# Performance work log

Hardware: AMD Instinct MI355X
Metric: run time of the kernel (lower is better)

The kernel has to match this reference:

```python
import jax, jax.numpy as jnp
import numpy as np

N_NODES = 50000
N_EDGES = 600000
D = 128
HIDDEN = 128
N_GRAPHS = 128
N_CLASSES = 10
N_STACKED = 3  # num_layers - 1


def setup_inputs() -> dict:
    key = jax.random.key(0)
    ks = jax.random.split(key, 12)
    s = 1.0 / np.sqrt(HIDDEN)
    inp = {
        "x": jax.random.normal(ks[0], (N_NODES, D), dtype=jnp.float32),
        "edge_index": jax.random.randint(ks[1], (2, N_EDGES), 0, N_NODES, dtype=jnp.int64),
        "batch": jnp.sort(jax.random.randint(ks[2], (N_NODES,), 0, N_GRAPHS, dtype=jnp.int64)),
        "W1": jax.random.normal(ks[3], (D, HIDDEN), dtype=jnp.float32) * s,
        "R1": jax.random.normal(ks[4], (D, HIDDEN), dtype=jnp.float32) * s,
        "b1": jnp.zeros((HIDDEN,), dtype=jnp.float32),
        "Wc": jax.random.normal(ks[5], (N_STACKED, HIDDEN, HIDDEN), dtype=jnp.float32) * s,
        "Rc": jax.random.normal(ks[6], (N_STACKED, HIDDEN, HIDDEN), dtype=jnp.float32) * s,
        "bc": jnp.zeros((N_STACKED, HIDDEN), dtype=jnp.float32),
        "lin1_w": jax.random.normal(ks[7], (HIDDEN, HIDDEN), dtype=jnp.float32) * s,
        "lin1_b": jnp.zeros((HIDDEN,), dtype=jnp.float32),
        "lin2_w": jax.random.normal(ks[8], (HIDDEN, N_CLASSES), dtype=jnp.float32) * s,
        "lin2_b": jnp.zeros((N_CLASSES,), dtype=jnp.float32),
    }
    return inp


def _gcn_norm(edge_index, n_nodes):
    # symmetric GCN normalization coeffs per edge (edge_weight=None -> ones)
    src, dst = edge_index[0], edge_index[1]
    ones = jnp.ones((edge_index.shape[1],), dtype=jnp.float32)
    deg = jax.ops.segment_sum(ones, dst, num_segments=n_nodes)
    dinv = jnp.where(deg > 0, jax.lax.rsqrt(jnp.maximum(deg, 1.0)), 0.0)
    return dinv[src] * dinv[dst]


def _gcs(x, src, dst, norm, W, R, b):
    # GCN aggregation on transformed features + linear skip (root) connection
    h = x @ W                                   # [N, H]
    msg = h[src] * norm[:, None]                # gather + scale, [E, H]
    agg = jax.ops.segment_sum(msg, dst, num_segments=x.shape[0])
    return agg + x @ R + b


def reference(x, edge_index, batch, W1, R1, b1, Wc, Rc, bc,
              lin1_w, lin1_b, lin2_w, lin2_b):
    src, dst = edge_index[0], edge_index[1]
    norm = _gcn_norm(edge_index, x.shape[0])

    h = jax.nn.relu(_gcs(x, src, dst, norm, W1, R1, b1))
    for i in range(N_STACKED):
        h = jax.nn.relu(_gcs(h, src, dst, norm, Wc[i], Rc[i], bc[i]))
    last = h

    # global mean pool over graphs
    sums = jax.ops.segment_sum(h, batch, num_segments=N_GRAPHS)
    cnts = jax.ops.segment_sum(jnp.ones((h.shape[0],), h.dtype), batch,
                               num_segments=N_GRAPHS)
    pooled = sums / jnp.maximum(cnts, 1.0)[:, None]

    g = jax.nn.relu(pooled @ lin1_w + lin1_b)   # dropout is identity in eval mode
    logits = g @ lin2_w + lin2_b
    return jax.nn.log_softmax(logits, axis=-1), last
```

## Files before the change

### kernel.cpp

```cpp
#include <hip/hip_runtime.h>

#define N_NODES  50000
#define N_EDGES  600000
#define DIM      128
#define N_GRAPHS 128
#define N_CLASSES 10
#define NB_SCAN  196
#define LDSW     136
#define NZB      8204


typedef __bf16 bf16x8 __attribute__((ext_vector_type(8)));
typedef float  f32x4  __attribute__((ext_vector_type(4)));

__device__ inline unsigned short f2bf(float f) {
  union { float f; unsigned int i; } u; u.f = f;
  unsigned int r = u.i + 0x7fff + ((u.i >> 16) & 1);
  return (unsigned short)(r >> 16);
}
__device__ inline float bf2f(unsigned short s) {
  union { unsigned int i; float f; } u; u.i = ((unsigned int)s) << 16;
  return u.f;
}
__device__ inline bf16x8 pack8(float4 lo, float4 hi) {
  union { bf16x8 v; unsigned short s[8]; } u;
  u.s[0] = f2bf(lo.x); u.s[1] = f2bf(lo.y); u.s[2] = f2bf(lo.z); u.s[3] = f2bf(lo.w);
  u.s[4] = f2bf(hi.x); u.s[5] = f2bf(hi.y); u.s[6] = f2bf(hi.z); u.s[7] = f2bf(hi.w);
  return u.v;
}


__global__ __launch_bounds__(256) void k_prep(float* __restrict__ zbase,
                                              const float* __restrict__ W1,
                                              const float* __restrict__ R1,
                                              const float* __restrict__ Wc,
                                              const float* __restrict__ Rc,
                                              unsigned short* __restrict__ pk) {
  if (blockIdx.x < NZB) {
    int i = blockIdx.x * 256 + threadIdx.x;
    if (i < 2100000) zbase[i] = 0.f;
    return;
  }
  int pb = blockIdx.x - NZB;
  int mm = pb >> 3, sub = pb & 7;
  const float* src = (mm == 0) ? W1
                   : (mm < 4)  ? Wc + (size_t)(mm - 1) * DIM * DIM
                   : (mm == 4) ? R1
                               : Rc + (size_t)(mm - 5) * DIM * DIM;
  int idx = sub * 256 + threadIdx.x;
  int lane = idx & 63;
  int kc   = (idx >> 6) & 3;
  int nt   = idx >> 8;
  int col  = nt * 16 + (lane & 15);
  int k0   = kc * 32 + (lane >> 4) * 8;
  unsigned short* dst = pk + (size_t)mm * 16384 + (size_t)idx * 8;
  ushort4 u;
  u.x = f2bf(src[(k0 + 0) * DIM + col]);
  u.y = f2bf(src[(k0 + 1) * DIM + col]);
  u.z = f2bf(src[(k0 + 2) * DIM + col]);
  u.w = f2bf(src[(k0 + 3) * DIM + col]);
  *(ushort4*)&dst[0] = u;
  u.x = f2bf(src[(k0 + 4) * DIM + col]);
  u.y = f2bf(src[(k0 + 5) * DIM + col]);
  u.z = f2bf(src[(k0 + 6) * DIM + col]);
  u.w = f2bf(src[(k0 + 7) * DIM + col]);
  *(ushort4*)&dst[4] = u;
}


__global__ __launch_bounds__(256) void k_deg(const int* __restrict__ ei,
                                             int* __restrict__ deg) {
  int e = blockIdx.x * 256 + threadIdx.x;
  if (e < N_EDGES) atomicAdd(&deg[ei[N_EDGES + e]], 1);
}

__global__ __launch_bounds__(256) void k_dinvsum(const int* __restrict__ deg,
                                                 float* __restrict__ dinv,
                                                 int* __restrict__ bsum) {
  int i = blockIdx.x * 256 + threadIdx.x;
  int t = threadIdx.x;
  int d = (i < N_NODES) ? deg[i] : 0;
  if (i < N_NODES) dinv[i] = (d > 0) ? rsqrtf((float)d) : 0.f;
  int dp = (d + 7) & ~7;
  __shared__ int tmp[256];
  tmp[t] = dp;
  __syncthreads();
  for (int off = 128; off > 0; off >>= 1) {
    if (t < off) tmp[t] += tmp[t + off];
    __syncthreads();
  }
  if (t == 0) bsum[blockIdx.x] = tmp[0];
}

__global__ __launch_bounds__(256) void k_bscan(const int* __restrict__ bsum,
                                               int* __restrict__ boff,
                                               int* __restrict__ rowp) {
  int t = threadIdx.x;
  int v = (t < NB_SCAN) ? bsum[t] : 0;
  __shared__ int tmp[256];
  tmp[t] = v;
  __syncthreads();
  for (int off = 1; off < 256; off <<= 1) {
    int add = (t >= off) ? tmp[t - off] : 0;
    __syncthreads();
    tmp[t] += add;
    __syncthreads();
  }
  boff[t] = tmp[t] - v;
  if (t == 255) rowp[N_NODES] = tmp[255];
}

__global__ __launch_bounds__(256) void k_rowp(const int* __restrict__ deg,
                                              const int* __restrict__ boff,
                                              int* __restrict__ rowp) {
  int i = blockIdx.x * 256 + threadIdx.x;
  int t = threadIdx.x;
  int dp = (i < N_NODES) ? ((deg[i] + 7) & ~7) : 0;
  __shared__ int tmp[256];
  tmp[t] = dp;
  __syncthreads();
  for (int off = 1; off < 256; off <<= 1) {
    int add = (t >= off) ? tmp[t - off] : 0;
    __syncthreads();
    tmp[t] += add;
    __syncthreads();
  }
  if (i < N_NODES) rowp[i] = boff[blockIdx.x] + tmp[t] - dp;
}

__global__ __launch_bounds__(256) void k_fill(const int* __restrict__ ei,
                                              const int* __restrict__ rowp,
                                              int* __restrict__ cnt,
                                              const float* __restrict__ dinv,
                                              int* __restrict__ csrc,
                                              float* __restrict__ enorm) {
  int e = blockIdx.x * 256 + threadIdx.x;
  if (e < N_EDGES) {
    int s = ei[e];
    int d = ei[N_EDGES + e];
    int p = rowp[d] + atomicAdd(&cnt[d], 1);
    csrc[p] = s;
    enorm[p] = dinv[s] * dinv[d];
  }
}


__global__ __launch_bounds__(256) void k_gemm0(const float* __restrict__ xf,
                                               const unsigned short* __restrict__ pkW,
                                               const unsigned short* __restrict__ pkR,
                                               const float* __restrict__ bv,
                                               unsigned short* __restrict__ hwb,
                                               unsigned short* __restrict__ skipb) {
  const int tid  = threadIdx.x;
  const int wave = tid >> 6, lane = tid & 63;
  const int m = lane & 15, q = lane >> 4;
  const int rbase = blockIdx.x * 64 + wave * 16;
  const int arow  = rbase + m;
  const bool aok  = arow < N_NODES;

  bf16x8 a[4];
#pragma unroll
  for (int kc = 0; kc < 4; ++kc) {
    float4 lo = make_float4(0.f, 0.f, 0.f, 0.f);
    float4 hi = make_float4(0.f, 0.f, 0.f, 0.f);
    if (aok) {
      lo = *(const float4*)&xf[arow * DIM + kc * 32 + q * 8];
      hi = *(const float4*)&xf[arow * DIM + kc * 32 + q * 8 + 4];
    }
    a[kc] = pack8(lo, hi);
  }

  f32x4 acc[16];
#pragma unroll
  for (int t = 0; t < 16; ++t) acc[t] = (f32x4){0.f, 0.f, 0.f, 0.f};

#pragma unroll
  for (int nt = 0; nt < 8; ++nt) {
    const unsigned short* pw = pkW + ((size_t)(nt * 4) * 64 + lane) * 8;
    const unsigned short* pr = pkR + ((size_t)(nt * 4) * 64 + lane) * 8;
#pragma unroll
    for (int kc = 0; kc < 4; ++kc) {
      bf16x8 bW = *(const bf16x8*)(pw + (size_t)kc * 64 * 8);
      acc[nt] = __builtin_amdgcn_mfma_f32_16x16x32_bf16(a[kc], bW, acc[nt], 0, 0, 0);
    }
#pragma unroll
    for (int kc = 0; kc < 4; ++kc) {
      bf16x8 bR = *(const bf16x8*)(pr + (size_t)kc * 64 * 8);
      acc[8 + nt] = __builtin_amdgcn_mfma_f32_16x16x32_bf16(a[kc], bR, acc[8 + nt], 0, 0, 0);
    }
  }

#pragma unroll
  for (int nt = 0; nt < 8; ++nt) {
    int col = nt * 16 + m;
    float bias = bv[col];
#pragma unroll
    for (int rg = 0; rg < 4; ++rg) {
      int row = rbase + q * 4 + rg;
      if (row < N_NODES) {
        hwb[row * DIM + col]   = f2bf(acc[nt][rg]);
        skipb[row * DIM + col] = f2bf(acc[8 + nt][rg] + bias);
      }
    }
  }
}


template<bool LAST>
__global__ __launch_bounds__(256) void k_aggemm(const unsigned short* __restrict__ hin,
                                                const int* __restrict__ rowp,
                                                const int* __restrict__ csrc,
                                                const float* __restrict__ enorm,
                                                const unsigned short* __restrict__ pkW,
                                                const unsigned short* __restrict__ pkR,
                                                const float* __restrict__ bv,
                                                unsigned short* __restrict__ hout,
                                                unsigned short* __restrict__ skipb,
                                                float* __restrict__ skipf) {
  __shared__ unsigned short xs[64 * LDSW];
  const int tid = threadIdx.x;
  const int row0 = blockIdx.x * 64;

  {
    int hw = tid >> 5;
    int l4 = (tid & 31) * 4;
    for (int rnd = 0; rnd < 8; ++rnd) {
      int n = row0 + rnd * 8 + hw;
      float4 acc = make_float4(0.f, 0.f, 0.f, 0.f);
      if (n < N_NODES) {
        ushort4 s = *(const ushort4*)&skipb[n * DIM + l4];
        acc = make_float4(bf2f(s.x), bf2f(s.y), bf2f(s.z), bf2f(s.w));
        int e0 = rowp[n], e1 = rowp[n + 1];
        for (int e = e0; e < e1; e += 8) {
          int4   csA = *(const int4*)&csrc[e];
          int4   csB = *(const int4*)&csrc[e + 4];
          float4 wvA = *(const float4*)&enorm[e];
          float4 wvB = *(const float4*)&enorm[e + 4];
          ushort4 u0 = *(const ushort4*)&hin[csA.x * DIM + l4];
          ushort4 u1 = *(const ushort4*)&hin[csA.y * DIM + l4];
          ushort4 u2 = *(const ushort4*)&hin[csA.z * DIM + l4];
          ushort4 u3 = *(const ushort4*)&hin[csA.w * DIM + l4];
          ushort4 u4 = *(const ushort4*)&hin[csB.x * DIM + l4];
          ushort4 u5 = *(const ushort4*)&hin[csB.y * DIM + l4];
          ushort4 u6 = *(const ushort4*)&hin[csB.z * DIM + l4];
          ushort4 u7 = *(const ushort4*)&hin[csB.w * DIM + l4];
          acc.x = fmaf(wvA.x, bf2f(u0.x), fmaf(wvA.y, bf2f(u1.x), fmaf(wvA.z, bf2f(u2.x), fmaf(wvA.w, bf2f(u3.x), acc.x))));
          acc.x = fmaf(wvB.x, bf2f(u4.x), fmaf(wvB.y, bf2f(u5.x), fmaf(wvB.z, bf2f(u6.x), fmaf(wvB.w, bf2f(u7.x), acc.x))));
          acc.y = fmaf(wvA.x, bf2f(u0.y), fmaf(wvA.y, bf2f(u1.y), fmaf(wvA.z, bf2f(u2.y), fmaf(wvA.w, bf2f(u3.y), acc.y))));
          acc.y = fmaf(wvB.x, bf2f(u4.y), fmaf(wvB.y, bf2f(u5.y), fmaf(wvB.z, bf2f(u6.y), fmaf(wvB.w, bf2f(u7.y), acc.y))));
          acc.z = fmaf(wvA.x, bf2f(u0.z), fmaf(wvA.y, bf2f(u1.z), fmaf(wvA.z, bf2f(u2.z), fmaf(wvA.w, bf2f(u3.z), acc.z))));
          acc.z = fmaf(wvB.x, bf2f(u4.z), fmaf(wvB.y, bf2f(u5.z), fmaf(wvB.z, bf2f(u6.z), fmaf(wvB.w, bf2f(u7.z), acc.z))));
          acc.w = fmaf(wvA.x, bf2f(u0.w), fmaf(wvA.y, bf2f(u1.w), fmaf(wvA.z, bf2f(u2.w), fmaf(wvA.w, bf2f(u3.w), acc.w))));
          acc.w = fmaf(wvB.x, bf2f(u4.w), fmaf(wvB.y, bf2f(u5.w), fmaf(wvB.z, bf2f(u6.w), fmaf(wvB.w, bf2f(u7.w), acc.w))));
        }
        acc.x = fmaxf(acc.x, 0.f);
        acc.y = fmaxf(acc.y, 0.f);
        acc.z = fmaxf(acc.z, 0.f);
        acc.w = fmaxf(acc.w, 0.f);
      }
      int r = rnd * 8 + hw;
      ushort4 o;
      o.x = f2bf(acc.x); o.y = f2bf(acc.y); o.z = f2bf(acc.z); o.w = f2bf(acc.w);
      *(ushort4*)&xs[r * LDSW + l4] = o;
    }
  }
  __syncthreads();

  const int wave = tid >> 6, lane = tid & 63;
  const int m = lane & 15, q = lane >> 4;
  const int rbase = row0 + wave * 16;

  bf16x8 a[4];
#pragma unroll
  for (int kc = 0; kc < 4; ++kc)
    a[kc] = *(const bf16x8*)&xs[(wave * 16 + m) * LDSW + kc * 32 + q * 8];

  f32x4 acc[16];
#pragma unroll
  for (int t = 0; t < 16; ++t) acc[t] = (f32x4){0.f, 0.f, 0.f, 0.f};

#pragma unroll
  for (int nt = 0; nt < 8; ++nt) {
    const unsigned short* pw = pkW + ((size_t)(nt * 4) * 64 + lane) * 8;
    const unsigned short* pr = pkR + ((size_t)(nt * 4) * 64 + lane) * 8;
#pragma unroll
    for (int kc = 0; kc < 4; ++kc) {
      bf16x8 bW = *(const bf16x8*)(pw + (size_t)kc * 64 * 8);
      acc[nt] = __builtin_amdgcn_mfma_f32_16x16x32_bf16(a[kc], bW, acc[nt], 0, 0, 0);
    }
#pragma unroll
    for (int kc = 0; kc < 4; ++kc) {
      bf16x8 bR = *(const bf16x8*)(pr + (size_t)kc * 64 * 8);
      acc[8 + nt] = __builtin_amdgcn_mfma_f32_16x16x32_bf16(a[kc], bR, acc[8 + nt], 0, 0, 0);
    }
  }

#pragma unroll
  for (int nt = 0; nt < 8; ++nt) {
    int col = nt * 16 + m;
    float bias = bv[col];
#pragma unroll
    for (int rg = 0; rg < 4; ++rg) {
      int row = rbase + q * 4 + rg;
      if (row < N_NODES) {
        hout[row * DIM + col] = f2bf(acc[nt][rg]);
        float v = acc[8 + nt][rg] + bias;
        if (LAST) skipf[row * DIM + col] = v;
        else      skipb[row * DIM + col] = f2bf(v);
      }
    }
  }
}


__global__ __launch_bounds__(256) void k_aggF(const unsigned short* __restrict__ hwb,
                                              const int* __restrict__ rowp,
                                              const int* __restrict__ csrc,
                                              const float* __restrict__ enorm,
                                              float* __restrict__ actf) {
  int n = blockIdx.x * 8 + (threadIdx.x >> 5);
  if (n >= N_NODES) return;
  int l4 = (threadIdx.x & 31) * 4;
  float4 acc = *(const float4*)&actf[n * DIM + l4];
  int e0 = rowp[n], e1 = rowp[n + 1];
  for (int e = e0; e < e1; e += 8) {
    int4   csA = *(const int4*)&csrc[e];
    int4   csB = *(const int4*)&csrc[e + 4];
    float4 wvA = *(const float4*)&enorm[e];
    float4 wvB = *(const float4*)&enorm[e + 4];
    ushort4 u0 = *(const ushort4*)&hwb[csA.x * DIM + l4];
    ushort4 u1 = *(const ushort4*)&hwb[csA.y * DIM + l4];
    ushort4 u2 = *(const ushort4*)&hwb[csA.z * DIM + l4];
    ushort4 u3 = *(const ushort4*)&hwb[csA.w * DIM + l4];
    ushort4 u4 = *(const ushort4*)&hwb[csB.x * DIM + l4];
    ushort4 u5 = *(const ushort4*)&hwb[csB.y * DIM + l4];
    ushort4 u6 = *(const ushort4*)&hwb[csB.z * DIM + l4];
    ushort4 u7 = *(const ushort4*)&hwb[csB.w * DIM + l4];
    acc.x = fmaf(wvA.x, bf2f(u0.x), fmaf(wvA.y, bf2f(u1.x), fmaf(wvA.z, bf2f(u2.x), fmaf(wvA.w, bf2f(u3.x), acc.x))));
    acc.x = fmaf(wvB.x, bf2f(u4.x), fmaf(wvB.y, bf2f(u5.x), fmaf(wvB.z, bf2f(u6.x), fmaf(wvB.w, bf2f(u7.x), acc.x))));
    acc.y = fmaf(wvA.x, bf2f(u0.y), fmaf(wvA.y, bf2f(u1.y), fmaf(wvA.z, bf2f(u2.y), fmaf(wvA.w, bf2f(u3.y), acc.y))));
    acc.y = fmaf(wvB.x, bf2f(u4.y), fmaf(wvB.y, bf2f(u5.y), fmaf(wvB.z, bf2f(u6.y), fmaf(wvB.w, bf2f(u7.y), acc.y))));
    acc.z = fmaf(wvA.x, bf2f(u0.z), fmaf(wvA.y, bf2f(u1.z), fmaf(wvA.z, bf2f(u2.z), fmaf(wvA.w, bf2f(u3.z), acc.z))));
    acc.z = fmaf(wvB.x, bf2f(u4.z), fmaf(wvB.y, bf2f(u5.z), fmaf(wvB.z, bf2f(u6.z), fmaf(wvB.w, bf2f(u7.z), acc.z))));
    acc.w = fmaf(wvA.x, bf2f(u0.w), fmaf(wvA.y, bf2f(u1.w), fmaf(wvA.z, bf2f(u2.w), fmaf(wvA.w, bf2f(u3.w), acc.w))));
    acc.w = fmaf(wvB.x, bf2f(u4.w), fmaf(wvB.y, bf2f(u5.w), fmaf(wvB.z, bf2f(u6.w), fmaf(wvB.w, bf2f(u7.w), acc.w))));
  }
  acc.x = fmaxf(acc.x, 0.f);
  acc.y = fmaxf(acc.y, 0.f);
  acc.z = fmaxf(acc.z, 0.f);
  acc.w = fmaxf(acc.w, 0.f);
  *(float4*)&actf[n * DIM + l4] = acc;
}


__global__ __launch_bounds__(1024) void k_pool2(const float* __restrict__ h,
                                                const int* __restrict__ batch,
                                                float* __restrict__ pooled) {
  int g = blockIdx.x;
  int t = threadIdx.x;
  __shared__ int sb[2];
  if (t < 2) {
    int target = g + t;
    int lo = 0, hi = N_NODES;
    while (lo < hi) {
      int mid = (lo + hi) >> 1;
      if (batch[mid] < target) lo = mid + 1; else hi = mid;
    }
    sb[t] = lo;
  }
  __syncthreads();
  int start = sb[0], end = sb[1];
  int c = t & 127, rg = t >> 7;
  float acc = 0.f;
  for (int r = start + rg; r < end; r += 8) acc += h[r * DIM + c];
  __shared__ float sp[8][DIM];
  sp[rg][c] = acc;
  __syncthreads();
  if (rg == 0) {
    float tot = acc;
#pragma unroll
    for (int i = 1; i < 8; ++i) tot += sp[i][c];
    float cnt = fmaxf((float)(end - start), 1.f);
    pooled[g * DIM + c] = tot / cnt;
  }
}


__global__ __launch_bounds__(128) void k_mlp1(const float* __restrict__ pooled,
                                              const float* __restrict__ w,
                                              const float* __restrict__ bias,
                                              float* __restrict__ g1) {
  int g = blockIdx.x, t = threadIdx.x;
  __shared__ float sp[DIM];
  sp[t] = pooled[g * DIM + t];
  __syncthreads();
  float acc = bias[t];
#pragma unroll 4
  for (int k = 0; k < DIM; ++k) acc = fmaf(sp[k], w[k * DIM + t], acc);
  g1[g * DIM + t] = fmaxf(acc, 0.f);
}

__global__ __launch_bounds__(128) void k_mlp2(const float* __restrict__ g1,
                                              const float* __restrict__ w,
                                              const float* __restrict__ bias,
                                              float* __restrict__ out) {
  int g = threadIdx.x;
  float l[N_CLASSES];
#pragma unroll
  for (int c = 0; c < N_CLASSES; ++c) l[c] = bias[c];
  for (int k = 0; k < DIM; ++k) {
    float gv = g1[g * DIM + k];
#pragma unroll
    for (int c = 0; c < N_CLASSES; ++c) l[c] = fmaf(gv, w[k * N_CLASSES + c], l[c]);
  }
  float m = l[0];
#pragma unroll
  for (int c = 1; c < N_CLASSES; ++c) m = fmaxf(m, l[c]);
  float s = 0.f;
#pragma unroll
  for (int c = 0; c < N_CLASSES; ++c) s += expf(l[c] - m);
  float lse = logf(s) + m;
#pragma unroll
  for (int c = 0; c < N_CLASSES; ++c) out[g * N_CLASSES + c] = l[c] - lse;
}


extern "C" void kernel_launch(void* const* d_in, const int* in_sizes, int n_in,
                              void* d_out, int out_size, void* d_ws, size_t ws_size,
                              hipStream_t stream) {
  const float* x     = (const float*)d_in[0];
  const int* ei      = (const int*)d_in[1];
  const int* batch   = (const int*)d_in[2];
  const float* W1  = (const float*)d_in[3];
  const float* R1  = (const float*)d_in[4];
  const float* b1  = (const float*)d_in[5];
  const float* Wc  = (const float*)d_in[6];
  const float* Rc  = (const float*)d_in[7];
  const float* bc  = (const float*)d_in[8];
  const float* l1w = (const float*)d_in[9];
  const float* l1b = (const float*)d_in[10];
  const float* l2w = (const float*)d_in[11];
  const float* l2b = (const float*)d_in[12];

  float* out   = (float*)d_out;
  float* dlast = out + N_GRAPHS * N_CLASSES;

  float* ws = (float*)d_ws;
  unsigned short* h0    = (unsigned short*)ws;
  unsigned short* h1    = (unsigned short*)(ws + 3200000);
  unsigned short* skipb = (unsigned short*)(ws + 6400000);
  int*   deg   = (int*)(ws + 9600000);
  int*   cnt   = (int*)(ws + 9650000);
  int*   csrc  = (int*)(ws + 9700000);
  float* enorm = ws + 10700000;
  float* dinv  = ws + 11700000;
  int*   rowp  = (int*)(ws + 11750000);
  float* pooled= ws + 11800016;
  float* g1    = ws + 11816400;
  unsigned short* pk = (unsigned short*)(ws + 11832784);
  int*   bsum  = (int*)(ws + 11898320);
  int*   boff  = (int*)(ws + 11898576);

  k_prep<<<NZB + 64, 256, 0, stream>>>(ws + 9600000, W1, R1, Wc, Rc, pk);
  k_deg <<<(N_EDGES + 255) / 256, 256, 0, stream>>>(ei, deg);
  k_dinvsum<<<NB_SCAN, 256, 0, stream>>>(deg, dinv, bsum);
  k_bscan<<<1, 256, 0, stream>>>(bsum, boff, rowp);
  k_rowp<<<NB_SCAN, 256, 0, stream>>>(deg, boff, rowp);
  k_fill<<<(N_EDGES + 255) / 256, 256, 0, stream>>>(ei, rowp, cnt, dinv, csrc, enorm);

  const int NGB = (N_NODES + 63) / 64;
  const int NAB = (N_NODES + 7) / 8;

  k_gemm0<<<NGB, 256, 0, stream>>>(x, pk + 0 * 16384, pk + 4 * 16384, b1, h0, skipb);
  k_aggemm<false><<<NGB, 256, 0, stream>>>(h0, rowp, csrc, enorm,
      pk + 1 * 16384, pk + 5 * 16384, bc + 0 * DIM, h1, skipb, nullptr);
  k_aggemm<false><<<NGB, 256, 0, stream>>>(h1, rowp, csrc, enorm,
      pk + 2 * 16384, pk + 6 * 16384, bc + 1 * DIM, h0, skipb, nullptr);
  k_aggemm<true><<<NGB, 256, 0, stream>>>(h0, rowp, csrc, enorm,
      pk + 3 * 16384, pk + 7 * 16384, bc + 2 * DIM, h1, skipb, dlast);
  k_aggF<<<NAB, 256, 0, stream>>>(h1, rowp, csrc, enorm, dlast);

  k_pool2<<<N_GRAPHS, 1024, 0, stream>>>(dlast, batch, pooled);
  k_mlp1<<<N_GRAPHS, 128, 0, stream>>>(pooled, l1w, l1b, g1);
  k_mlp2<<<1, N_GRAPHS, 0, stream>>>(g1, l2w, l2b, out);
}
```

Measured before the change: 400.8 us.

## Pack edge src and norm into int2 and split aggemm GEMM paths across waves

```diff
diff --git a/kernel.cpp b/kernel.cpp
--- a/kernel.cpp
+++ b/kernel.cpp
@@ -132,15 +132,13 @@
                                               const int* __restrict__ rowp,
                                               int* __restrict__ cnt,
                                               const float* __restrict__ dinv,
-                                              int* __restrict__ csrc,
-                                              float* __restrict__ enorm) {
+                                              int2* __restrict__ epk) {
   int e = blockIdx.x * 256 + threadIdx.x;
   if (e < N_EDGES) {
     int s = ei[e];
     int d = ei[N_EDGES + e];
     int p = rowp[d] + atomicAdd(&cnt[d], 1);
-    csrc[p] = s;
-    enorm[p] = dinv[s] * dinv[d];
+    epk[p] = make_int2(s, __float_as_int(dinv[s] * dinv[d]));
   }
 }
 
@@ -207,10 +205,9 @@
 
 
 template<bool LAST>
-__global__ __launch_bounds__(256) void k_aggemm(const unsigned short* __restrict__ hin,
+__global__ __launch_bounds__(512) void k_aggemm(const unsigned short* __restrict__ hin,
                                                 const int* __restrict__ rowp,
-                                                const int* __restrict__ csrc,
-                                                const float* __restrict__ enorm,
+                                                const int2* __restrict__ epk,
                                                 const unsigned short* __restrict__ pkW,
                                                 const unsigned short* __restrict__ pkR,
                                                 const float* __restrict__ bv,
@@ -224,41 +221,45 @@
   {
     int hw = tid >> 5;
     int l4 = (tid & 31) * 4;
-    for (int rnd = 0; rnd < 8; ++rnd) {
-      int n = row0 + rnd * 8 + hw;
+    for (int rnd = 0; rnd < 4; ++rnd) {
+      int n = row0 + rnd * 16 + hw;
       float4 acc = make_float4(0.f, 0.f, 0.f, 0.f);
       if (n < N_NODES) {
         ushort4 s = *(const ushort4*)&skipb[n * DIM + l4];
         acc = make_float4(bf2f(s.x), bf2f(s.y), bf2f(s.z), bf2f(s.w));
         int e0 = rowp[n], e1 = rowp[n + 1];
         for (int e = e0; e < e1; e += 8) {
-          int4   csA = *(const int4*)&csrc[e];
-          int4   csB = *(const int4*)&csrc[e + 4];
-          float4 wvA = *(const float4*)&enorm[e];
-          float4 wvB = *(const float4*)&enorm[e + 4];
-          ushort4 u0 = *(const ushort4*)&hin[csA.x * DIM + l4];
-          ushort4 u1 = *(const ushort4*)&hin[csA.y * DIM + l4];
-          ushort4 u2 = *(const ushort4*)&hin[csA.z * DIM + l4];
-          ushort4 u3 = *(const ushort4*)&hin[csA.w * DIM + l4];
-          ushort4 u4 = *(const ushort4*)&hin[csB.x * DIM + l4];
-          ushort4 u5 = *(const ushort4*)&hin[csB.y * DIM + l4];
-          ushort4 u6 = *(const ushort4*)&hin[csB.z * DIM + l4];
-          ushort4 u7 = *(const ushort4*)&hin[csB.w * DIM + l4];
-          acc.x = fmaf(wvA.x, bf2f(u0.x), fmaf(wvA.y, bf2f(u1.x), fmaf(wvA.z, bf2f(u2.x), fmaf(wvA.w, bf2f(u3.x), acc.x))));
-          acc.x = fmaf(wvB.x, bf2f(u4.x), fmaf(wvB.y, bf2f(u5.x), fmaf(wvB.z, bf2f(u6.x), fmaf(wvB.w, bf2f(u7.x), acc.x))));
-          acc.y = fmaf(wvA.x, bf2f(u0.y), fmaf(wvA.y, bf2f(u1.y), fmaf(wvA.z, bf2f(u2.y), fmaf(wvA.w, bf2f(u3.y), acc.y))));
-          acc.y = fmaf(wvB.x, bf2f(u4.y), fmaf(wvB.y, bf2f(u5.y), fmaf(wvB.z, bf2f(u6.y), fmaf(wvB.w, bf2f(u7.y), acc.y))));
-          acc.z = fmaf(wvA.x, bf2f(u0.z), fmaf(wvA.y, bf2f(u1.z), fmaf(wvA.z, bf2f(u2.z), fmaf(wvA.w, bf2f(u3.z), acc.z))));
-          acc.z = fmaf(wvB.x, bf2f(u4.z), fmaf(wvB.y, bf2f(u5.z), fmaf(wvB.z, bf2f(u6.z), fmaf(wvB.w, bf2f(u7.z), acc.z))));
-          acc.w = fmaf(wvA.x, bf2f(u0.w), fmaf(wvA.y, bf2f(u1.w), fmaf(wvA.z, bf2f(u2.w), fmaf(wvA.w, bf2f(u3.w), acc.w))));
-          acc.w = fmaf(wvB.x, bf2f(u4.w), fmaf(wvB.y, bf2f(u5.w), fmaf(wvB.z, bf2f(u6.w), fmaf(wvB.w, bf2f(u7.w), acc.w))));
+          int4 p0 = *(const int4*)&epk[e];
+          int4 p1 = *(const int4*)&epk[e + 2];
+          int4 p2 = *(const int4*)&epk[e + 4];
+          int4 p3 = *(const int4*)&epk[e + 6];
+          ushort4 u0 = *(const ushort4*)&hin[p0.x * DIM + l4];
+          ushort4 u1 = *(const ushort4*)&hin[p0.z * DIM + l4];
+          ushort4 u2 = *(const ushort4*)&hin[p1.x * DIM + l4];
+          ushort4 u3 = *(const ushort4*)&hin[p1.z * DIM + l4];
+          ushort4 u4 = *(const ushort4*)&hin[p2.x * DIM + l4];
+          ushort4 u5 = *(const ushort4*)&hin[p2.z * DIM + l4];
+          ushort4 u6 = *(const ushort4*)&hin[p3.x * DIM + l4];
+          ushort4 u7 = *(const ushort4*)&hin[p3.z * DIM + l4];
+          float w0 = __int_as_float(p0.y), w1 = __int_as_float(p0.w);
+          float w2 = __int_as_float(p1.y), w3 = __int_as_float(p1.w);
+          float w4 = __int_as_float(p2.y), w5 = __int_as_float(p2.w);
+          float w6 = __int_as_float(p3.y), w7 = __int_as_float(p3.w);
+          acc.x = fmaf(w0, bf2f(u0.x), fmaf(w1, bf2f(u1.x), fmaf(w2, bf2f(u2.x), fmaf(w3, bf2f(u3.x), acc.x))));
+          acc.x = fmaf(w4, bf2f(u4.x), fmaf(w5, bf2f(u5.x), fmaf(w6, bf2f(u6.x), fmaf(w7, bf2f(u7.x), acc.x))));
+          acc.y = fmaf(w0, bf2f(u0.y), fmaf(w1, bf2f(u1.y), fmaf(w2, bf2f(u2.y), fmaf(w3, bf2f(u3.y), acc.y))));
+          acc.y = fmaf(w4, bf2f(u4.y), fmaf(w5, bf2f(u5.y), fmaf(w6, bf2f(u6.y), fmaf(w7, bf2f(u7.y), acc.y))));
+          acc.z = fmaf(w0, bf2f(u0.z), fmaf(w1, bf2f(u1.z), fmaf(w2, bf2f(u2.z), fmaf(w3, bf2f(u3.z), acc.z))));
+          acc.z = fmaf(w4, bf2f(u4.z), fmaf(w5, bf2f(u5.z), fmaf(w6, bf2f(u6.z), fmaf(w7, bf2f(u7.z), acc.z))));
+          acc.w = fmaf(w0, bf2f(u0.w), fmaf(w1, bf2f(u1.w), fmaf(w2, bf2f(u2.w), fmaf(w3, bf2f(u3.w), acc.w))));
+          acc.w = fmaf(w4, bf2f(u4.w), fmaf(w5, bf2f(u5.w), fmaf(w6, bf2f(u6.w), fmaf(w7, bf2f(u7.w), acc.w))));
         }
         acc.x = fmaxf(acc.x, 0.f);
         acc.y = fmaxf(acc.y, 0.f);
         acc.z = fmaxf(acc.z, 0.f);
         acc.w = fmaxf(acc.w, 0.f);
       }
-      int r = rnd * 8 + hw;
+      int r = rnd * 16 + hw;
       ushort4 o;
       o.x = f2bf(acc.x); o.y = f2bf(acc.y); o.z = f2bf(acc.z); o.w = f2bf(acc.w);
       *(ushort4*)&xs[r * LDSW + l4] = o;
@@ -267,46 +268,53 @@
   __syncthreads();
 
   const int wave = tid >> 6, lane = tid & 63;
+  const int rt = wave & 3, path = wave >> 2;
   const int m = lane & 15, q = lane >> 4;
-  const int rbase = row0 + wave * 16;
+  const int rbase = row0 + rt * 16;
+  const unsigned short* pkM = path ? pkR : pkW;
 
   bf16x8 a[4];
 #pragma unroll
   for (int kc = 0; kc < 4; ++kc)
-    a[kc] = *(const bf16x8*)&xs[(wave * 16 + m) * LDSW + kc * 32 + q * 8];
-
-  f32x4 acc[16];
-#pragma unroll
-  for (int t = 0; t < 16; ++t) acc[t] = (f32x4){0.f, 0.f, 0.f, 0.f};
+    a[kc] = *(const bf16x8*)&xs[(rt * 16 + m) * LDSW + kc * 32 + q * 8];
+
+  f32x4 acc[8];
+#pragma unroll
+  for (int t = 0; t < 8; ++t) acc[t] = (f32x4){0.f, 0.f, 0.f, 0.f};
 
 #pragma unroll
   for (int nt = 0; nt < 8; ++nt) {
-    const unsigned short* pw = pkW + ((size_t)(nt * 4) * 64 + lane) * 8;
-    const unsigned short* pr = pkR + ((size_t)(nt * 4) * 64 + lane) * 8;
+    const unsigned short* pm = pkM + ((size_t)(nt * 4) * 64 + lane) * 8;
 #pragma unroll
     for (int kc = 0; kc < 4; ++kc) {
-      bf16x8 bW = *(const bf16x8*)(pw + (size_t)kc * 64 * 8);
-      acc[nt] = __builtin_amdgcn_mfma_f32_16x16x32_bf16(a[kc], bW, acc[nt], 0, 0, 0);
-    }
-#pragma unroll
-    for (int kc = 0; kc < 4; ++kc) {
-      bf16x8 bR = *(const bf16x8*)(pr + (size_t)kc * 64 * 8);
-      acc[8 + nt] = __builtin_amdgcn_mfma_f32_16x16x32_bf16(a[kc], bR, acc[8 + nt], 0, 0, 0);
-    }
-  }
-
-#pragma unroll
-  for (int nt = 0; nt < 8; ++nt) {
-    int col = nt * 16 + m;
-    float bias = bv[col];
-#pragma unroll
-    for (int rg = 0; rg < 4; ++rg) {
-      int row = rbase + q * 4 + rg;
-      if (row < N_NODES) {
-        hout[row * DIM + col] = f2bf(acc[nt][rg]);
-        float v = acc[8 + nt][rg] + bias;
-        if (LAST) skipf[row * DIM + col] = v;
-        else      skipb[row * DIM + col] = f2bf(v);
+      bf16x8 b = *(const bf16x8*)(pm + (size_t)kc * 64 * 8);
+      acc[nt] = __builtin_amdgcn_mfma_f32_16x16x32_bf16(a[kc], b, acc[nt], 0, 0, 0);
+    }
+  }
+
+  if (path == 0) {
+#pragma unroll
+    for (int nt = 0; nt < 8; ++nt) {
+      int col = nt * 16 + m;
+#pragma unroll
+      for (int rg = 0; rg < 4; ++rg) {
+        int row = rbase + q * 4 + rg;
+        if (row < N_NODES) hout[row * DIM + col] = f2bf(acc[nt][rg]);
+      }
+    }
+  } else {
+#pragma unroll
+    for (int nt = 0; nt < 8; ++nt) {
+      int col = nt * 16 + m;
+      float bias = bv[col];
+#pragma unroll
+      for (int rg = 0; rg < 4; ++rg) {
+        int row = rbase + q * 4 + rg;
+        if (row < N_NODES) {
+          float v = acc[nt][rg] + bias;
+          if (LAST) skipf[row * DIM + col] = v;
+          else      skipb[row * DIM + col] = f2bf(v);
+        }
       }
     }
   }
@@ -315,8 +323,7 @@
 
 __global__ __launch_bounds__(256) void k_aggF(const unsigned short* __restrict__ hwb,
                                               const int* __restrict__ rowp,
-                                              const int* __restrict__ csrc,
-                                              const float* __restrict__ enorm,
+                                              const int2* __restrict__ epk,
                                               float* __restrict__ actf) {
   int n = blockIdx.x * 8 + (threadIdx.x >> 5);
   if (n >= N_NODES) return;
@@ -324,26 +331,30 @@
   float4 acc = *(const float4*)&actf[n * DIM + l4];
   int e0 = rowp[n], e1 = rowp[n + 1];
   for (int e = e0; e < e1; e += 8) {
-    int4   csA = *(const int4*)&csrc[e];
-    int4   csB = *(const int4*)&csrc[e + 4];
-    float4 wvA = *(const float4*)&enorm[e];
-    float4 wvB = *(const float4*)&enorm[e + 4];
-    ushort4 u0 = *(const ushort4*)&hwb[csA.x * DIM + l4];
-    ushort4 u1 = *(const ushort4*)&hwb[csA.y * DIM + l4];
-    ushort4 u2 = *(const ushort4*)&hwb[csA.z * DIM + l4];
-    ushort4 u3 = *(const ushort4*)&hwb[csA.w * DIM + l4];
-    ushort4 u4 = *(const ushort4*)&hwb[csB.x * DIM + l4];
-    ushort4 u5 = *(const ushort4*)&hwb[csB.y * DIM + l4];
-    ushort4 u6 = *(const ushort4*)&hwb[csB.z * DIM + l4];
-    ushort4 u7 = *(const ushort4*)&hwb[csB.w * DIM + l4];
-    acc.x = fmaf(wvA.x, bf2f(u0.x), fmaf(wvA.y, bf2f(u1.x), fmaf(wvA.z, bf2f(u2.x), fmaf(wvA.w, bf2f(u3.x), acc.x))));
-    acc.x = fmaf(wvB.x, bf2f(u4.x), fmaf(wvB.y, bf2f(u5.x), fmaf(wvB.z, bf2f(u6.x), fmaf(wvB.w, bf2f(u7.x), acc.x))));
-    acc.y = fmaf(wvA.x, bf2f(u0.y), fmaf(wvA.y, bf2f(u1.y), fmaf(wvA.z, bf2f(u2.y), fmaf(wvA.w, bf2f(u3.y), acc.y))));
-    acc.y = fmaf(wvB.x, bf2f(u4.y), fmaf(wvB.y, bf2f(u5.y), fmaf(wvB.z, bf2f(u6.y), fmaf(wvB.w, bf2f(u7.y), acc.y))));
-    acc.z = fmaf(wvA.x, bf2f(u0.z), fmaf(wvA.y, bf2f(u1.z), fmaf(wvA.z, bf2f(u2.z), fmaf(wvA.w, bf2f(u3.z), acc.z))));
-    acc.z = fmaf(wvB.x, bf2f(u4.z), fmaf(wvB.y, bf2f(u5.z), fmaf(wvB.z, bf2f(u6.z), fmaf(wvB.w, bf2f(u7.z), acc.z))));
-    acc.w = fmaf(wvA.x, bf2f(u0.w), fmaf(wvA.y, bf2f(u1.w), fmaf(wvA.z, bf2f(u2.w), fmaf(wvA.w, bf2f(u3.w), acc.w))));
-    acc.w = fmaf(wvB.x, bf2f(u4.w), fmaf(wvB.y, bf2f(u5.w), fmaf(wvB.z, bf2f(u6.w), fmaf(wvB.w, bf2f(u7.w), acc.w))));
+    int4 p0 = *(const int4*)&epk[e];
+    int4 p1 = *(const int4*)&epk[e + 2];
+    int4 p2 = *(const int4*)&epk[e + 4];
+    int4 p3 = *(const int4*)&epk[e + 6];
+    ushort4 u0 = *(const ushort4*)&hwb[p0.x * DIM + l4];
+    ushort4 u1 = *(const ushort4*)&hwb[p0.z * DIM + l4];
+    ushort4 u2 = *(const ushort4*)&hwb[p1.x * DIM + l4];
+    ushort4 u3 = *(const ushort4*)&hwb[p1.z * DIM + l4];
+    ushort4 u4 = *(const ushort4*)&hwb[p2.x * DIM + l4];
+    ushort4 u5 = *(const ushort4*)&hwb[p2.z * DIM + l4];
+    ushort4 u6 = *(const ushort4*)&hwb[p3.x * DIM + l4];
+    ushort4 u7 = *(const ushort4*)&hwb[p3.z * DIM + l4];
+    float w0 = __int_as_float(p0.y), w1 = __int_as_float(p0.w);
+    float w2 = __int_as_float(p1.y), w3 = __int_as_float(p1.w);
+    float w4 = __int_as_float(p2.y), w5 = __int_as_float(p2.w);
+    float w6 = __int_as_float(p3.y), w7 = __int_as_float(p3.w);
+    acc.x = fmaf(w0, bf2f(u0.x), fmaf(w1, bf2f(u1.x), fmaf(w2, bf2f(u2.x), fmaf(w3, bf2f(u3.x), acc.x))));
+    acc.x = fmaf(w4, bf2f(u4.x), fmaf(w5, bf2f(u5.x), fmaf(w6, bf2f(u6.x), fmaf(w7, bf2f(u7.x), acc.x))));
+    acc.y = fmaf(w0, bf2f(u0.y), fmaf(w1, bf2f(u1.y), fmaf(w2, bf2f(u2.y), fmaf(w3, bf2f(u3.y), acc.y))));
+    acc.y = fmaf(w4, bf2f(u4.y), fmaf(w5, bf2f(u5.y), fmaf(w6, bf2f(u6.y), fmaf(w7, bf2f(u7.y), acc.y))));
+    acc.z = fmaf(w0, bf2f(u0.z), fmaf(w1, bf2f(u1.z), fmaf(w2, bf2f(u2.z), fmaf(w3, bf2f(u3.z), acc.z))));
+    acc.z = fmaf(w4, bf2f(u4.z), fmaf(w5, bf2f(u5.z), fmaf(w6, bf2f(u6.z), fmaf(w7, bf2f(u7.z), acc.z))));
+    acc.w = fmaf(w0, bf2f(u0.w), fmaf(w1, bf2f(u1.w), fmaf(w2, bf2f(u2.w), fmaf(w3, bf2f(u3.w), acc.w))));
+    acc.w = fmaf(w4, bf2f(u4.w), fmaf(w5, bf2f(u5.w), fmaf(w6, bf2f(u6.w), fmaf(w7, bf2f(u7.w), acc.w))));
   }
   acc.x = fmaxf(acc.x, 0.f);
   acc.y = fmaxf(acc.y, 0.f);
@@ -451,8 +462,7 @@
   unsigned short* skipb = (unsigned short*)(ws + 6400000);
   int*   deg   = (int*)(ws + 9600000);
   int*   cnt   = (int*)(ws + 9650000);
-  int*   csrc  = (int*)(ws + 9700000);
-  float* enorm = ws + 10700000;
+  int2*  epk   = (int2*)(ws + 9700000);
   float* dinv  = ws + 11700000;
   int*   rowp  = (int*)(ws + 11750000);
   float* pooled= ws + 11800016;
@@ -466,19 +476,19 @@
   k_dinvsum<<<NB_SCAN, 256, 0, stream>>>(deg, dinv, bsum);
   k_bscan<<<1, 256, 0, stream>>>(bsum, boff, rowp);
   k_rowp<<<NB_SCAN, 256, 0, stream>>>(deg, boff, rowp);
-  k_fill<<<(N_EDGES + 255) / 256, 256, 0, stream>>>(ei, rowp, cnt, dinv, csrc, enorm);
+  k_fill<<<(N_EDGES + 255) / 256, 256, 0, stream>>>(ei, rowp, cnt, dinv, epk);
 
   const int NGB = (N_NODES + 63) / 64;
   const int NAB = (N_NODES + 7) / 8;
 
   k_gemm0<<<NGB, 256, 0, stream>>>(x, pk + 0 * 16384, pk + 4 * 16384, b1, h0, skipb);
-  k_aggemm<false><<<NGB, 256, 0, stream>>>(h0, rowp, csrc, enorm,
+  k_aggemm<false><<<NGB, 512, 0, stream>>>(h0, rowp, epk,
       pk + 1 * 16384, pk + 5 * 16384, bc + 0 * DIM, h1, skipb, nullptr);
-  k_aggemm<false><<<NGB, 256, 0, stream>>>(h1, rowp, csrc, enorm,
+  k_aggemm<false><<<NGB, 512, 0, stream>>>(h1, rowp, epk,
       pk + 2 * 16384, pk + 6 * 16384, bc + 1 * DIM, h0, skipb, nullptr);
-  k_aggemm<true><<<NGB, 256, 0, stream>>>(h0, rowp, csrc, enorm,
+  k_aggemm<true><<<NGB, 512, 0, stream>>>(h0, rowp, epk,
       pk + 3 * 16384, pk + 7 * 16384, bc + 2 * DIM, h1, skipb, dlast);
-  k_aggF<<<NAB, 256, 0, stream>>>(h1, rowp, csrc, enorm, dlast);
+  k_aggF<<<NAB, 256, 0, stream>>>(h1, rowp, epk, dlast);
 
   k_pool2<<<N_GRAPHS, 1024, 0, stream>>>(dlast, batch, pooled);
   k_mlp1<<<N_GRAPHS, 128, 0, stream>>>(pooled, l1w, l1b, g1);
```

Measured after the change: 405.7 us. About the same (+1.2%).
